# Kernel tuning notes

Measured on AMD Instinct MI355X. Metric: run time of the kernel, lower is better.

## Reference

```python
import jax, jax.numpy as jnp
import numpy as np

EMBED_DIM = 1024
B, C, H, W = 32, 1024, 32, 32


def _conv1x1(x, w, b):
    # x: [B,C,H,W], w: [O,C] (squeezed 1x1 conv kernel), b: [O]
    return jnp.einsum('bchw,oc->bohw', x, w) + b[None, :, None, None]


def setup_inputs() -> dict:
    key = jax.random.key(0)
    ks = jax.random.split(key, 12)
    s = 1.0 / np.sqrt(C)  # torch Conv2d default init scale (uniform bound)
    inp = {
        'shape_map': jax.random.normal(ks[0], (B, C, H, W), jnp.float32),
        'img_map': jax.random.normal(ks[1], (B, C, H, W), jnp.float32),
        'wq': jax.random.uniform(ks[2], (C, C), jnp.float32, -s, s),
        'bq': jax.random.uniform(ks[3], (C,), jnp.float32, -s, s),
        'wk': jax.random.uniform(ks[4], (C, C), jnp.float32, -s, s),
        'bk': jax.random.uniform(ks[5], (C,), jnp.float32, -s, s),
        'wv': jax.random.uniform(ks[6], (C, C), jnp.float32, -s, s),
        'bv': jax.random.uniform(ks[7], (C,), jnp.float32, -s, s),
        'wc': jax.random.uniform(ks[8], (C, C), jnp.float32, -s, s),
        'bc': jax.random.uniform(ks[9], (C,), jnp.float32, -s, s),
    }
    return inp


def reference(shape_map, img_map, wq, bq, wk, bk, wv, bv, wc, bc):
    # QKV embeddings: 1x1 conv + tanh (dropout is identity at inference)
    q = jnp.tanh(_conv1x1(shape_map, wq, bq))  # [B,C,H,W]
    k = jnp.tanh(_conv1x1(img_map, wk, bk))
    v = jnp.tanh(_conv1x1(img_map, wv, bv))

    hw = H * W
    q_flat = q.reshape(B, C, hw)
    k_flat = k.reshape(B, C, hw)
    v_flat = v.reshape(B, C, hw)

    # channel-attention: scores over channel pairs, contracted over spatial HW
    scores = jnp.einsum('bcs,bds->bcd', q_flat, k_flat) / jnp.sqrt(
        jnp.asarray(C, q_flat.dtype))  # [B,C,C]
    weights = jax.nn.softmax(scores, axis=-1)
    new_v = jnp.einsum('bcd,bds->bcs', weights, v_flat).reshape(B, C, H, W)

    out = _conv1x1(new_v, wc, bc) + shape_map
    return out
```

## Files before the change

kernel.cpp:

```cpp
#include <hip/hip_runtime.h>


typedef __bf16 bf16x8 __attribute__((ext_vector_type(8)));
typedef float floatx4 __attribute__((ext_vector_type(4)));

__device__ __forceinline__ unsigned short f2bf(float f) {
  union { float f; unsigned int u; } c; c.f = f;
  unsigned int u = c.u;
  u += 0x7fffu + ((u >> 16) & 1u);
  return (unsigned short)(u >> 16);
}

__device__ __forceinline__ float tanh_fast(float x) {
  x = fminf(15.0f, fmaxf(-15.0f, x));
  float t = __expf(2.0f * x);
  return (t - 1.0f) / (t + 1.0f);
}

template<int OUT_F32, int BIAS_MODE ,
         int TANH_ON, int RESID_ON>
__global__ __launch_bounds__(256, 2)
void gemm_bt(const unsigned short* __restrict__ A,
             const unsigned short* __restrict__ B,
             void* __restrict__ Cv,
             const float* __restrict__ bias,
             const float* __restrict__ resid,
             float scale,
             size_t sA, size_t sB, size_t sC, size_t sR)
{
  constexpr int K = 1024;
  const unsigned short* Ab = A + blockIdx.z * sA;
  const unsigned short* Bb = B + blockIdx.z * sB;

  __shared__ unsigned short lA[128 * 32];
  __shared__ unsigned short lB[128 * 32];

  const int tid  = threadIdx.x;
  const int w    = tid >> 6;
  const int lane = tid & 63;
  const int quad = lane >> 4;
  const int lm   = lane & 15;
  const int wm   = (w >> 1) * 64;
  const int wn   = (w & 1) * 64;
  const int m0 = blockIdx.y * 128, n0 = blockIdx.x * 128;

  const int srow = lane >> 2;
  const int scol = (lane & 3) * 8;

  floatx4 acc[4][4];
#pragma unroll
  for (int i = 0; i < 4; ++i)
#pragma unroll
    for (int j = 0; j < 4; ++j)
      acc[i][j] = (floatx4)(0.0f);

  const unsigned short* gA0 = Ab + (size_t)(m0 + srow) * K + scol;
  const unsigned short* gB0 = Bb + (size_t)(n0 + srow) * K + scol;

  for (int k0 = 0; k0 < K; k0 += 32) {
#pragma unroll
    for (int i = 0; i < 2; ++i) {
      const int q = w * 2 + i;
      __builtin_amdgcn_global_load_lds(
          (__attribute__((address_space(1))) void*)(gA0 + (size_t)q * 16 * K + k0),
          (__attribute__((address_space(3))) void*)(&lA[q * 512]), 16, 0, 0);
      __builtin_amdgcn_global_load_lds(
          (__attribute__((address_space(1))) void*)(gB0 + (size_t)q * 16 * K + k0),
          (__attribute__((address_space(3))) void*)(&lB[q * 512]), 16, 0, 0);
    }
    __syncthreads();

    bf16x8 af[4], bfv[4];
#pragma unroll
    for (int i = 0; i < 4; ++i)
      af[i] = *(const bf16x8*)(&lA[(wm + 16 * i + lm) * 32 + quad * 8]);
#pragma unroll
    for (int j = 0; j < 4; ++j)
      bfv[j] = *(const bf16x8*)(&lB[(wn + 16 * j + lm) * 32 + quad * 8]);

#pragma unroll
    for (int i = 0; i < 4; ++i)
#pragma unroll
      for (int j = 0; j < 4; ++j)
        acc[i][j] = __builtin_amdgcn_mfma_f32_16x16x32_bf16(
            af[i], bfv[j], acc[i][j], 0, 0, 0);

    __syncthreads();
  }

  float* Cf = (float*)Cv + blockIdx.z * sC;
  unsigned short* Cb = (unsigned short*)Cv + blockIdx.z * sC;
  const float* rp = RESID_ON ? (resid + blockIdx.z * sR) : (const float*)0;

#pragma unroll
  for (int i = 0; i < 4; ++i) {
    const int mbase = m0 + wm + 16 * i + quad * 4;
#pragma unroll
    for (int j = 0; j < 4; ++j) {
      const int n = n0 + wn + 16 * j + lm;
#pragma unroll
      for (int r = 0; r < 4; ++r) {
        const int m = mbase + r;
        float val = acc[i][j][r] * scale;
        if (BIAS_MODE == 1) val += bias[m];
        if (BIAS_MODE == 2) val += bias[n];
        if (TANH_ON) val = tanh_fast(val);
        if (RESID_ON) val += rp[(size_t)m * 1024 + n];
        if (OUT_F32) Cf[(size_t)m * 1024 + n] = val;
        else         Cb[(size_t)m * 1024 + n] = f2bf(val);
      }
    }
  }
}

__global__ __launch_bounds__(256)
void transpose_cvt(const float* __restrict__ in, unsigned short* __restrict__ out,
                   size_t sIn, size_t sOut)
{
  __shared__ float tile[32][33];
  in  += blockIdx.z * sIn;
  out += blockIdx.z * sOut;
  const int x  = blockIdx.x * 32 + threadIdx.x;
  const int y0 = blockIdx.y * 32;
#pragma unroll
  for (int k = 0; k < 32; k += 8)
    tile[threadIdx.y + k][threadIdx.x] =
        in[(size_t)(y0 + threadIdx.y + k) * 1024 + x];
  __syncthreads();
  const int xo  = blockIdx.y * 32 + threadIdx.x;
  const int yo0 = blockIdx.x * 32;
#pragma unroll
  for (int k = 0; k < 32; k += 8)
    out[(size_t)(yo0 + threadIdx.y + k) * 1024 + xo] =
        f2bf(tile[threadIdx.x][threadIdx.y + k]);
}

__global__ __launch_bounds__(256)
void softmax_rows(const float* __restrict__ S, unsigned short* __restrict__ W,
                  size_t sS, size_t sW)
{
  const float* s = S + blockIdx.y * sS + (size_t)blockIdx.x * 1024;
  unsigned short* w = W + blockIdx.y * sW + (size_t)blockIdx.x * 1024;
  const int t = threadIdx.x;
  float4 v = ((const float4*)s)[t];
  float mx = fmaxf(fmaxf(v.x, v.y), fmaxf(v.z, v.w));
#pragma unroll
  for (int off = 32; off > 0; off >>= 1)
    mx = fmaxf(mx, __shfl_xor(mx, off));
  __shared__ float redm[4], reds[4];
  const int lane = t & 63, wv = t >> 6;
  if (lane == 0) redm[wv] = mx;
  __syncthreads();
  mx = fmaxf(fmaxf(redm[0], redm[1]), fmaxf(redm[2], redm[3]));
  float e0 = __expf(v.x - mx), e1 = __expf(v.y - mx),
        e2 = __expf(v.z - mx), e3 = __expf(v.w - mx);
  float sum = e0 + e1 + e2 + e3;
#pragma unroll
  for (int off = 32; off > 0; off >>= 1)
    sum += __shfl_xor(sum, off);
  if (lane == 0) reds[wv] = sum;
  __syncthreads();
  sum = reds[0] + reds[1] + reds[2] + reds[3];
  const float inv = 1.0f / sum;
  w[4 * t + 0] = f2bf(e0 * inv);
  w[4 * t + 1] = f2bf(e1 * inv);
  w[4 * t + 2] = f2bf(e2 * inv);
  w[4 * t + 3] = f2bf(e3 * inv);
}

__global__ __launch_bounds__(256)
void cvt_w(const float* __restrict__ in, unsigned short* __restrict__ out)
{
  const int i = blockIdx.x * 256 + threadIdx.x;
  float4 v = ((const float4*)in)[i];
  ushort4 o;
  o.x = f2bf(v.x); o.y = f2bf(v.y); o.z = f2bf(v.z); o.w = f2bf(v.w);
  ((ushort4*)out)[i] = o;
}

extern "C" void kernel_launch(void* const* d_in, const int* in_sizes, int n_in,
                              void* d_out, int out_size, void* d_ws, size_t ws_size,
                              hipStream_t stream)
{
  const float* shape_map = (const float*)d_in[0];
  const float* img_map   = (const float*)d_in[1];
  const float* wq = (const float*)d_in[2];
  const float* bq = (const float*)d_in[3];
  const float* wk = (const float*)d_in[4];
  const float* bk = (const float*)d_in[5];
  const float* wv = (const float*)d_in[6];
  const float* bv = (const float*)d_in[7];
  const float* wc = (const float*)d_in[8];
  const float* bc = (const float*)d_in[9];
  float* out = (float*)d_out;

  const size_t ELT = 1024 * 1024;
  const size_t MB  = 1024 * 1024;
  char* ws = (char*)d_ws;

  unsigned short* wq_b = (unsigned short*)(ws + 0 * 2 * MB);
  unsigned short* wk_b = (unsigned short*)(ws + 1 * 2 * MB);
  unsigned short* wv_b = (unsigned short*)(ws + 2 * 2 * MB);
  unsigned short* wc_b = (unsigned short*)(ws + 3 * 2 * MB);
  char* slots = ws + 8 * MB;
  const size_t slotBytes = 10 * MB;
  int nslots = (ws_size > 8 * MB + slotBytes)
                   ? (int)((ws_size - 8 * MB) / slotBytes) : 1;
  if (nslots > 32) nslots = 32;
  if (nslots < 1)  nslots = 1;

  cvt_w<<<1024, 256, 0, stream>>>(wq, wq_b);
  cvt_w<<<1024, 256, 0, stream>>>(wk, wk_b);
  cvt_w<<<1024, 256, 0, stream>>>(wv, wv_b);
  cvt_w<<<1024, 256, 0, stream>>>(wc, wc_b);

  const size_t sBf = slotBytes / 2;
  const size_t sF  = slotBytes / 4;

  for (int c0 = 0; c0 < 32; c0 += nslots) {
    const int nb = (32 - c0 < nslots) ? (32 - c0) : nslots;

    unsigned short* Xt  = (unsigned short*)(slots + 0);
    unsigned short* Yt  = (unsigned short*)(slots + 2 * MB);
    float*          Sm  = (float*)(slots + 0);
    unsigned short* Qb  = (unsigned short*)(slots + 4 * MB);
    unsigned short* Kb  = (unsigned short*)(slots + 6 * MB);
    unsigned short* Vt  = (unsigned short*)(slots + 8 * MB);
    unsigned short* Wsm = Qb;
    unsigned short* NVt = Kb;

    dim3 tgrid(32, 32, nb), tblk(32, 8);
    transpose_cvt<<<tgrid, tblk, 0, stream>>>(shape_map + (size_t)c0 * ELT, Xt, ELT, sBf);
    transpose_cvt<<<tgrid, tblk, 0, stream>>>(img_map   + (size_t)c0 * ELT, Yt, ELT, sBf);

    dim3 ggrid(8, 8, nb);
    gemm_bt<0, 1, 1, 0><<<ggrid, 256, 0, stream>>>(
        wq_b, Xt, Qb, bq, nullptr, 1.0f, 0, sBf, sBf, 0);
    gemm_bt<0, 1, 1, 0><<<ggrid, 256, 0, stream>>>(
        wk_b, Yt, Kb, bk, nullptr, 1.0f, 0, sBf, sBf, 0);
    gemm_bt<0, 2, 1, 0><<<ggrid, 256, 0, stream>>>(
        Yt, wv_b, Vt, bv, nullptr, 1.0f, sBf, 0, sBf, 0);
    gemm_bt<1, 0, 0, 0><<<ggrid, 256, 0, stream>>>(
        Qb, Kb, Sm, nullptr, nullptr, 0.03125f, sBf, sBf, sF, 0);
    softmax_rows<<<dim3(1024, nb), 256, 0, stream>>>(Sm, Wsm, sF, sBf);
    gemm_bt<0, 0, 0, 0><<<ggrid, 256, 0, stream>>>(
        Vt, Wsm, NVt, nullptr, nullptr, 1.0f, sBf, sBf, sBf, 0);
    gemm_bt<1, 1, 0, 1><<<ggrid, 256, 0, stream>>>(
        wc_b, NVt, out + (size_t)c0 * ELT, bc,
        shape_map + (size_t)c0 * ELT, 1.0f, 0, sBf, ELT, ELT);
  }
}
```

Before: 1.020 ms.

## Deepen GEMM K-tile with XOR-swizzled LDS and batch QKV/transpose/convert launches

The GEMM core now loads 64-wide K tiles instead of 32, which halves the number of barrier pairs per K loop. It stores them in LDS with an XOR swizzle to avoid bank conflicts on the fragment reads. The three Q/K/V projection GEMMs are merged into one launch indexed by grid z, and the two transposes and four weight conversions are each merged into single launches. This cuts launch overhead and fills more CUs per launch, at the cost of doubled LDS per block (32KB), which may limit occupancy.

```diff
diff --git a/kernel.cpp b/kernel.cpp
--- a/kernel.cpp
+++ b/kernel.cpp
@@ -17,8 +17,66 @@
   return (t - 1.0f) / (t + 1.0f);
 }
 
-template<int OUT_F32, int BIAS_MODE ,
-         int TANH_ON, int RESID_ON>
+__device__ __forceinline__ void gemm_core(
+    const unsigned short* __restrict__ Ab,
+    const unsigned short* __restrict__ Bb,
+    int m0, int n0,
+    unsigned short* lA, unsigned short* lB,
+    floatx4 acc[4][4])
+{
+  constexpr int K = 1024;
+  const int tid  = threadIdx.x;
+  const int w    = tid >> 6;
+  const int lane = tid & 63;
+  const int quad = lane >> 4;
+  const int lm   = lane & 15;
+  const int wm   = (w >> 1) * 64;
+  const int wn   = (w & 1) * 64;
+  const int xr   = lm & 7;
+
+  const int srow = lane >> 3;
+  const int sg   = (lane & 7) ^ srow;
+  const unsigned short* gA0 = Ab + (size_t)(m0 + srow) * K + sg * 8;
+  const unsigned short* gB0 = Bb + (size_t)(n0 + srow) * K + sg * 8;
+
+  for (int k0 = 0; k0 < K; k0 += 64) {
+#pragma unroll
+    for (int i = 0; i < 4; ++i) {
+      const int q = w * 4 + i;
+      __builtin_amdgcn_global_load_lds(
+          (__attribute__((address_space(1))) void*)(gA0 + (size_t)q * 8 * K + k0),
+          (__attribute__((address_space(3))) void*)(lA + q * 512), 16, 0, 0);
+      __builtin_amdgcn_global_load_lds(
+          (__attribute__((address_space(1))) void*)(gB0 + (size_t)q * 8 * K + k0),
+          (__attribute__((address_space(3))) void*)(lB + q * 512), 16, 0, 0);
+    }
+    __syncthreads();
+
+#pragma unroll
+    for (int ks = 0; ks < 2; ++ks) {
+      bf16x8 af[4], bfv[4];
+#pragma unroll
+      for (int i = 0; i < 4; ++i) {
+        const int row = wm + 16 * i + lm;
+        af[i] = *(const bf16x8*)(lA + row * 64 + (((ks * 4 + quad) ^ xr) * 8));
+      }
+#pragma unroll
+      for (int j = 0; j < 4; ++j) {
+        const int row = wn + 16 * j + lm;
+        bfv[j] = *(const bf16x8*)(lB + row * 64 + (((ks * 4 + quad) ^ xr) * 8));
+      }
+#pragma unroll
+      for (int i = 0; i < 4; ++i)
+#pragma unroll
+        for (int j = 0; j < 4; ++j)
+          acc[i][j] = __builtin_amdgcn_mfma_f32_16x16x32_bf16(
+              af[i], bfv[j], acc[i][j], 0, 0, 0);
+    }
+    __syncthreads();
+  }
+}
+
+template<int OUT_F32, int BIAS_MODE , int TANH_ON, int RESID_ON>
 __global__ __launch_bounds__(256, 2)
 void gemm_bt(const unsigned short* __restrict__ A,
              const unsigned short* __restrict__ B,
@@ -28,65 +86,20 @@
              float scale,
              size_t sA, size_t sB, size_t sC, size_t sR)
 {
-  constexpr int K = 1024;
-  const unsigned short* Ab = A + blockIdx.z * sA;
-  const unsigned short* Bb = B + blockIdx.z * sB;
-
-  __shared__ unsigned short lA[128 * 32];
-  __shared__ unsigned short lB[128 * 32];
-
-  const int tid  = threadIdx.x;
-  const int w    = tid >> 6;
-  const int lane = tid & 63;
-  const int quad = lane >> 4;
-  const int lm   = lane & 15;
-  const int wm   = (w >> 1) * 64;
-  const int wn   = (w & 1) * 64;
+  __shared__ unsigned short lA[128 * 64];
+  __shared__ unsigned short lB[128 * 64];
   const int m0 = blockIdx.y * 128, n0 = blockIdx.x * 128;
-
-  const int srow = lane >> 2;
-  const int scol = (lane & 3) * 8;
+  const int lane = threadIdx.x & 63, w = threadIdx.x >> 6;
+  const int quad = lane >> 4, lm = lane & 15;
+  const int wm = (w >> 1) * 64, wn = (w & 1) * 64;
 
   floatx4 acc[4][4];
 #pragma unroll
   for (int i = 0; i < 4; ++i)
 #pragma unroll
-    for (int j = 0; j < 4; ++j)
-      acc[i][j] = (floatx4)(0.0f);
-
-  const unsigned short* gA0 = Ab + (size_t)(m0 + srow) * K + scol;
-  const unsigned short* gB0 = Bb + (size_t)(n0 + srow) * K + scol;
-
-  for (int k0 = 0; k0 < K; k0 += 32) {
-#pragma unroll
-    for (int i = 0; i < 2; ++i) {
-      const int q = w * 2 + i;
-      __builtin_amdgcn_global_load_lds(
-          (__attribute__((address_space(1))) void*)(gA0 + (size_t)q * 16 * K + k0),
-          (__attribute__((address_space(3))) void*)(&lA[q * 512]), 16, 0, 0);
-      __builtin_amdgcn_global_load_lds(
-          (__attribute__((address_space(1))) void*)(gB0 + (size_t)q * 16 * K + k0),
-          (__attribute__((address_space(3))) void*)(&lB[q * 512]), 16, 0, 0);
-    }
-    __syncthreads();
-
-    bf16x8 af[4], bfv[4];
-#pragma unroll
-    for (int i = 0; i < 4; ++i)
-      af[i] = *(const bf16x8*)(&lA[(wm + 16 * i + lm) * 32 + quad * 8]);
-#pragma unroll
-    for (int j = 0; j < 4; ++j)
-      bfv[j] = *(const bf16x8*)(&lB[(wn + 16 * j + lm) * 32 + quad * 8]);
-
-#pragma unroll
-    for (int i = 0; i < 4; ++i)
-#pragma unroll
-      for (int j = 0; j < 4; ++j)
-        acc[i][j] = __builtin_amdgcn_mfma_f32_16x16x32_bf16(
-            af[i], bfv[j], acc[i][j], 0, 0, 0);
-
-    __syncthreads();
-  }
+    for (int j = 0; j < 4; ++j) acc[i][j] = (floatx4)(0.0f);
+
+  gemm_core(A + blockIdx.z * sA, B + blockIdx.z * sB, m0, n0, lA, lB, acc);
 
   float* Cf = (float*)Cv + blockIdx.z * sC;
   unsigned short* Cb = (unsigned short*)Cv + blockIdx.z * sC;
@@ -113,13 +126,79 @@
   }
 }
 
+__global__ __launch_bounds__(256, 2)
+void qkv_gemm(const unsigned short* __restrict__ wqb,
+              const unsigned short* __restrict__ wkb,
+              const unsigned short* __restrict__ wvb,
+              const unsigned short* __restrict__ Xt,
+              const unsigned short* __restrict__ Yt,
+              unsigned short* __restrict__ Qb,
+              unsigned short* __restrict__ Kb,
+              unsigned short* __restrict__ Vt,
+              const float* __restrict__ bq,
+              const float* __restrict__ bk,
+              const float* __restrict__ bv,
+              size_t sBf, int nb)
+{
+  __shared__ unsigned short lA[128 * 64];
+  __shared__ unsigned short lB[128 * 64];
+  const int z = blockIdx.z;
+  int op, b;
+  if (z >= 2 * nb)      { op = 2; b = z - 2 * nb; }
+  else if (z >= nb)     { op = 1; b = z - nb; }
+  else                  { op = 0; b = z; }
+
+  const unsigned short *A, *B;
+  unsigned short* C;
+  const float* bias;
+  int biasM;
+  if (op == 0)      { A = wqb;            B = Xt + b * sBf; C = Qb + b * sBf; bias = bq; biasM = 1; }
+  else if (op == 1) { A = wkb;            B = Yt + b * sBf; C = Kb + b * sBf; bias = bk; biasM = 1; }
+  else              { A = Yt + b * sBf;   B = wvb;          C = Vt + b * sBf; bias = bv; biasM = 0; }
+
+  const int m0 = blockIdx.y * 128, n0 = blockIdx.x * 128;
+  const int lane = threadIdx.x & 63, w = threadIdx.x >> 6;
+  const int quad = lane >> 4, lm = lane & 15;
+  const int wm = (w >> 1) * 64, wn = (w & 1) * 64;
+
+  floatx4 acc[4][4];
+#pragma unroll
+  for (int i = 0; i < 4; ++i)
+#pragma unroll
+    for (int j = 0; j < 4; ++j) acc[i][j] = (floatx4)(0.0f);
+
+  gemm_core(A, B, m0, n0, lA, lB, acc);
+
+#pragma unroll
+  for (int i = 0; i < 4; ++i) {
+    const int mbase = m0 + wm + 16 * i + quad * 4;
+#pragma unroll
+    for (int j = 0; j < 4; ++j) {
+      const int n = n0 + wn + 16 * j + lm;
+      const float bn = biasM ? 0.0f : bias[n];
+#pragma unroll
+      for (int r = 0; r < 4; ++r) {
+        const int m = mbase + r;
+        float val = acc[i][j][r] + (biasM ? bias[m] : bn);
+        val = tanh_fast(val);
+        C[(size_t)m * 1024 + n] = f2bf(val);
+      }
+    }
+  }
+}
+
 __global__ __launch_bounds__(256)
-void transpose_cvt(const float* __restrict__ in, unsigned short* __restrict__ out,
-                   size_t sIn, size_t sOut)
+void transpose2(const float* __restrict__ in0, const float* __restrict__ in1,
+                unsigned short* __restrict__ out0, unsigned short* __restrict__ out1,
+                size_t sIn, size_t sOut, int nb)
 {
   __shared__ float tile[32][33];
-  in  += blockIdx.z * sIn;
-  out += blockIdx.z * sOut;
+  const int z = blockIdx.z;
+  const float* in;
+  unsigned short* out;
+  if (z < nb) { in = in0 + (size_t)z * sIn;        out = out0 + (size_t)z * sOut; }
+  else        { in = in1 + (size_t)(z - nb) * sIn; out = out1 + (size_t)(z - nb) * sOut; }
+
   const int x  = blockIdx.x * 32 + threadIdx.x;
   const int y0 = blockIdx.y * 32;
 #pragma unroll
@@ -169,8 +248,18 @@
 }
 
 __global__ __launch_bounds__(256)
-void cvt_w(const float* __restrict__ in, unsigned short* __restrict__ out)
-{
+void cvt_all(const float* __restrict__ s0, const float* __restrict__ s1,
+             const float* __restrict__ s2, const float* __restrict__ s3,
+             unsigned short* __restrict__ d0, unsigned short* __restrict__ d1,
+             unsigned short* __restrict__ d2, unsigned short* __restrict__ d3)
+{
+  const float* in; unsigned short* out;
+  switch (blockIdx.y) {
+    case 0: in = s0; out = d0; break;
+    case 1: in = s1; out = d1; break;
+    case 2: in = s2; out = d2; break;
+    default: in = s3; out = d3; break;
+  }
   const int i = blockIdx.x * 256 + threadIdx.x;
   float4 v = ((const float4*)in)[i];
   ushort4 o;
@@ -209,10 +298,8 @@
   if (nslots > 32) nslots = 32;
   if (nslots < 1)  nslots = 1;
 
-  cvt_w<<<1024, 256, 0, stream>>>(wq, wq_b);
-  cvt_w<<<1024, 256, 0, stream>>>(wk, wk_b);
-  cvt_w<<<1024, 256, 0, stream>>>(wv, wv_b);
-  cvt_w<<<1024, 256, 0, stream>>>(wc, wc_b);
+  cvt_all<<<dim3(1024, 4), 256, 0, stream>>>(wq, wk, wv, wc,
+                                             wq_b, wk_b, wv_b, wc_b);
 
   const size_t sBf = slotBytes / 2;
   const size_t sF  = slotBytes / 4;
@@ -229,23 +316,22 @@
     unsigned short* Wsm = Qb;
     unsigned short* NVt = Kb;
 
-    dim3 tgrid(32, 32, nb), tblk(32, 8);
-    transpose_cvt<<<tgrid, tblk, 0, stream>>>(shape_map + (size_t)c0 * ELT, Xt, ELT, sBf);
-    transpose_cvt<<<tgrid, tblk, 0, stream>>>(img_map   + (size_t)c0 * ELT, Yt, ELT, sBf);
-
-    dim3 ggrid(8, 8, nb);
-    gemm_bt<0, 1, 1, 0><<<ggrid, 256, 0, stream>>>(
-        wq_b, Xt, Qb, bq, nullptr, 1.0f, 0, sBf, sBf, 0);
-    gemm_bt<0, 1, 1, 0><<<ggrid, 256, 0, stream>>>(
-        wk_b, Yt, Kb, bk, nullptr, 1.0f, 0, sBf, sBf, 0);
-    gemm_bt<0, 2, 1, 0><<<ggrid, 256, 0, stream>>>(
-        Yt, wv_b, Vt, bv, nullptr, 1.0f, sBf, 0, sBf, 0);
-    gemm_bt<1, 0, 0, 0><<<ggrid, 256, 0, stream>>>(
+    transpose2<<<dim3(32, 32, 2 * nb), dim3(32, 8), 0, stream>>>(
+        shape_map + (size_t)c0 * ELT, img_map + (size_t)c0 * ELT,
+        Xt, Yt, ELT, sBf, nb);
+
+    qkv_gemm<<<dim3(8, 8, 3 * nb), 256, 0, stream>>>(
+        wq_b, wk_b, wv_b, Xt, Yt, Qb, Kb, Vt, bq, bk, bv, sBf, nb);
+
+    gemm_bt<1, 0, 0, 0><<<dim3(8, 8, nb), 256, 0, stream>>>(
         Qb, Kb, Sm, nullptr, nullptr, 0.03125f, sBf, sBf, sF, 0);
+
     softmax_rows<<<dim3(1024, nb), 256, 0, stream>>>(Sm, Wsm, sF, sBf);
-    gemm_bt<0, 0, 0, 0><<<ggrid, 256, 0, stream>>>(
+
+    gemm_bt<0, 0, 0, 0><<<dim3(8, 8, nb), 256, 0, stream>>>(
         Vt, Wsm, NVt, nullptr, nullptr, 1.0f, sBf, sBf, sBf, 0);
-    gemm_bt<1, 1, 0, 1><<<ggrid, 256, 0, stream>>>(
+
+    gemm_bt<1, 1, 0, 1><<<dim3(8, 8, nb), 256, 0, stream>>>(
         wc_b, NVt, out + (size_t)c0 * ELT, bc,
         shape_map + (size_t)c0 * ELT, 1.0f, 0, sBf, ELT, ELT);
   }
```

New measurement: 1.011 ms. About the same (-0.9%).
